# Optimization experiments

Measured on AMD Instinct MI355X. Metric: run time of the kernel, lower is better.

## Reference

```python
import jax, jax.numpy as jnp
import numpy as np

# Phi-2 config
B, S = 4, 1024            # batch, seq_len (uniform prefill)
T = B * S                 # total tokens
HID = 2560
H = 32                    # attention heads
D = HID // H              # head_size = 80
ROT = int(0.4 * D)        # partial rotary dim = 32
THETA = 10000.0
SCALE = D ** -0.5
NUM_SLOTS = 2 * T


def setup_inputs() -> dict:
    key = jax.random.key(0)
    ks = jax.random.split(key, 6)
    hidden_states = jax.random.normal(ks[0], (T, HID), jnp.float32) * 0.02
    # true rope tables: positions restart per sequence
    pos = jnp.tile(jnp.arange(S, dtype=jnp.float32), B)                 # [T]
    inv_freq = 1.0 / (THETA ** (jnp.arange(0, ROT, 2, dtype=jnp.float32) / ROT))  # [ROT/2]
    freqs = pos[:, None] * inv_freq[None, :]                            # [T, ROT/2]
    cos, sin = jnp.cos(freqs), jnp.sin(freqs)
    slots = jnp.arange(T, dtype=jnp.int32)
    kv_cache_k = jnp.zeros((NUM_SLOTS, H, D), jnp.float32)
    kv_cache_v = jnp.zeros((NUM_SLOTS, H, D), jnp.float32)
    qkv_w = jax.random.normal(ks[1], (3 * HID, HID), jnp.float32) * 0.02
    qkv_b = jax.random.normal(ks[2], (3 * HID,), jnp.float32) * 0.02
    dense_w = jax.random.normal(ks[3], (HID, HID), jnp.float32) * 0.02
    dense_b = jax.random.normal(ks[4], (HID,), jnp.float32) * 0.02
    return {"hidden_states": hidden_states, "cos": cos, "sin": sin, "slots": slots,
            "kv_cache_k": kv_cache_k, "kv_cache_v": kv_cache_v,
            "qkv_w": qkv_w, "qkv_b": qkv_b, "dense_w": dense_w, "dense_b": dense_b}


def _partial_rope(x, cos, sin):
    # x: [T, H, D]; rotate-half rope on the first ROT dims only
    x1 = x[..., : ROT // 2]
    x2 = x[..., ROT // 2 : ROT]
    c = cos[:, None, :]  # [T,1,ROT/2]
    s = sin[:, None, :]
    rot = jnp.concatenate([x1 * c - x2 * s, x1 * s + x2 * c], axis=-1)
    return jnp.concatenate([rot, x[..., ROT:]], axis=-1)


def reference(hidden_states, cos, sin, slots, kv_cache_k, kv_cache_v,
              qkv_w, qkv_b, dense_w, dense_b):
    # fused QKV projection
    qkv = hidden_states @ qkv_w.T + qkv_b                 # [T, 3*HID]
    q = qkv[:, :HID].reshape(T, H, D)
    k = qkv[:, HID:2 * HID].reshape(T, H, D)
    v = qkv[:, 2 * HID:].reshape(T, H, D)
    # partial rotary on q and k
    q = _partial_rope(q, cos, sin)
    k = _partial_rope(k, cos, sin)
    # KV-cache write (reshape_and_cache)
    kc = kv_cache_k.at[slots].set(k)
    vc = kv_cache_v.at[slots].set(v)
    # causal flash-attention (prefill path), uniform seq lengths
    qb = q.reshape(B, S, H, D)
    kb = k.reshape(B, S, H, D)
    vb = v.reshape(B, S, H, D)
    scores = jnp.einsum("bqhd,bkhd->bhqk", qb, kb) * SCALE  # [B,H,S,S]
    causal = jnp.tril(jnp.ones((S, S), bool))
    scores = jnp.where(causal[None, None], scores, jnp.finfo(scores.dtype).min)
    probs = jax.nn.softmax(scores, axis=-1)
    attn = jnp.einsum("bhqk,bkhd->bqhd", probs, vb).reshape(T, HID)
    out = attn @ dense_w.T + dense_b                       # [T, HID]
    return out, kc, vc
```

## Files before the change

### kernel.cpp

```cpp
#include <hip/hip_runtime.h>

#define SEQ    1024
#define NBAT   4
#define TTOK   4096
#define HIDN   2560
#define NQKV   7680
#define NHEAD  32
#define DHEAD  80
#define NSLOT  8192
#define SCALE_F 0.111803398874989485f
#define LOG2E_F 1.4426950408889634f

typedef float  f32x4  __attribute__((ext_vector_type(4)));
typedef __bf16 bf16x8 __attribute__((ext_vector_type(8)));
typedef short  s16x8  __attribute__((ext_vector_type(8)));
typedef short  s16x4  __attribute__((ext_vector_type(4)));
typedef ushort u16x4  __attribute__((ext_vector_type(4)));

typedef __attribute__((address_space(3))) void lds_v;
typedef __attribute__((address_space(1))) void glb_v;

__device__ __forceinline__ void gload16(const void* g, void* l) {
  __builtin_amdgcn_global_load_lds((glb_v*)g, (lds_v*)l, 16, 0, 0);
}

__device__ __forceinline__ f32x4 mfma16(s16x8 a, s16x8 b, f32x4 c) {
  return __builtin_amdgcn_mfma_f32_16x16x32_bf16(
      __builtin_bit_cast(bf16x8, a), __builtin_bit_cast(bf16x8, b), c, 0, 0, 0);
}

__device__ __forceinline__ ushort f2bf(float f) {
  uint u = __builtin_bit_cast(uint, f);
  u += 0x7fffu + ((u >> 16) & 1u);
  return (ushort)(u >> 16);
}
__device__ __forceinline__ float bf2f(ushort h) {
  uint u = (uint)h << 16;
  return __builtin_bit_cast(float, u);
}

#define NQ_HS  2621440
#define NQ_QW  4915200
#define NQ_DW  1638400
#define NQ_ALL (NQ_HS + NQ_QW + NQ_DW)
__global__ __launch_bounds__(256)
void prep_kernel(const float* __restrict__ hs, const float* __restrict__ qkvw,
                 const float* __restrict__ densew,
                 ushort* __restrict__ hsb, ushort* __restrict__ qkvwb,
                 ushort* __restrict__ densewb, uint* __restrict__ flags) {
  const int tid0 = blockIdx.x * 256 + threadIdx.x;
  if (tid0 < NSLOT) flags[tid0] = 0u;
  const int stride = gridDim.x * 256;
  for (int i = tid0; i < NQ_ALL; i += stride) {
    const float* src; ushort* dst; int q;
    if (i < NQ_HS)              { src = hs;     dst = hsb;     q = i; }
    else if (i < NQ_HS + NQ_QW) { src = qkvw;   dst = qkvwb;   q = i - NQ_HS; }
    else                        { src = densew; dst = densewb; q = i - NQ_HS - NQ_QW; }
    float4 v = *(const float4*)(src + q * 4);
    u16x4 o = { f2bf(v.x), f2bf(v.y), f2bf(v.z), f2bf(v.w) };
    *(u16x4*)(dst + q * 4) = o;
  }
}

template<int OUT_BF16>
__global__ __launch_bounds__(512, 2)
void gemm8p(const ushort* __restrict__ A, const ushort* __restrict__ B,
            const float* __restrict__ bias, void* __restrict__ Cout,
            int M, int N, int K, int GX, int RR, int RC) {
  __shared__ ushort sA[3][256 * 64];
  __shared__ ushort sB[2][256 * 64];
  const int tid = threadIdx.x;
  const int l   = tid & 63;
  const int w   = tid >> 6;
  const int wm  = w >> 2, wn = w & 3;
  const int r   = l & 15,  g = l >> 4;

  const int fl  = blockIdx.x;
  const int xcd = fl & 7;
  const int idx = fl >> 3;
  const int cgroups = GX / RC;
  const int rg = xcd / cgroups, cg = xcd % cgroups;
  const int by = rg * RR + idx / RC;
  const int bx = cg * RC + idx % RC;
  const int m0  = by * 256, n0 = bx * 256;
  const int NT  = K >> 6;

  const int srow = w * 16 + (l >> 3);
  const int scol = ((l & 7) ^ (l >> 3)) * 8;
  const ushort* Ab = A + (size_t)(m0 + srow) * K + scol;
  const ushort* Bb = B + (size_t)(n0 + srow) * K + scol;
  const size_t r8   = (size_t)8 * K;
  const size_t r128 = (size_t)128 * K;

#define STG_A(t_, h_, buf_) { \
    const ushort* gp = Ab + (size_t)(t_) * 64 + (size_t)(h_) * r128; \
    char* lp = (char*)(&sA[buf_][0]) + ((h_) * 128 + w * 16) * 128; \
    gload16(gp, lp); gload16(gp + r8, lp + 1024); }
#define STG_B(t_, h_, buf_) { \
    const ushort* gp = Bb + (size_t)(t_) * 64 + (size_t)(h_) * r128; \
    char* lp = (char*)(&sB[buf_][0]) + ((h_) * 128 + w * 16) * 128; \
    gload16(gp, lp); gload16(gp + r8, lp + 1024); }

  const int kswz = (r & 7) * 8;
  const int c0 = (g * 8) ^ kswz;
  const int c1 = (32 + g * 8) ^ kswz;
  const int arow = (wm * 128 + r) * 64;
  const int brow = (wn * 64 + r) * 64;

  f32x4 acc[8][4];
#pragma unroll
  for (int m = 0; m < 8; m++)
#pragma unroll
    for (int n = 0; n < 4; n++) { f32x4 z = {0.f,0.f,0.f,0.f}; acc[m][n] = z; }

  STG_A(0, 0, 0); STG_A(0, 1, 0);
  STG_B(0, 0, 0); STG_B(0, 1, 0);
  STG_A(1, 0, 1); STG_A(1, 1, 1);
  asm volatile("s_waitcnt vmcnt(4)" ::: "memory");
  __builtin_amdgcn_sched_barrier(0);
  __builtin_amdgcn_s_barrier();

#define MFMA_Q(q_) \
    __builtin_amdgcn_s_setprio(1); \
    _Pragma("unroll") \
    for (int n = 0; n < 4; n++) acc[2*(q_)  ][n] = mfma16(x0, b0[n], acc[2*(q_)  ][n]); \
    _Pragma("unroll") \
    for (int n = 0; n < 4; n++) acc[2*(q_)+1][n] = mfma16(y0, b0[n], acc[2*(q_)+1][n]); \
    _Pragma("unroll") \
    for (int n = 0; n < 4; n++) acc[2*(q_)  ][n] = mfma16(x1, b1[n], acc[2*(q_)  ][n]); \
    _Pragma("unroll") \
    for (int n = 0; n < 4; n++) acc[2*(q_)+1][n] = mfma16(y1, b1[n], acc[2*(q_)+1][n]); \
    __builtin_amdgcn_s_setprio(0);

#define LOAD_A(m0_, m1_) \
    x0 = *(const s16x8*)&cA[arow + (m0_) * 1024 + c0]; \
    x1 = *(const s16x8*)&cA[arow + (m0_) * 1024 + c1]; \
    y0 = *(const s16x8*)&cA[arow + (m1_) * 1024 + c0]; \
    y1 = *(const s16x8*)&cA[arow + (m1_) * 1024 + c1];

  int bA = 0;
#pragma unroll 1
  for (int t = 0; t < NT; ++t) {
    const ushort* cA = &sA[bA][0];
    const ushort* cB = &sB[t & 1][0];
    const int nb = (t & 1) ^ 1;
    int a2 = bA + 2; if (a2 >= 3) a2 -= 3;

    s16x8 b0[4], b1[4], x0, x1, y0, y1;

#pragma unroll
    for (int n = 0; n < 4; n++) {
      b0[n] = *(const s16x8*)&cB[brow + n * 1024 + c0];
      b1[n] = *(const s16x8*)&cB[brow + n * 1024 + c1];
    }
    LOAD_A(0, 1)
    if (t + 1 < NT) STG_B(t + 1, 0, nb);
    __builtin_amdgcn_s_barrier();
    MFMA_Q(0)
    __builtin_amdgcn_s_barrier();

    LOAD_A(2, 3)
    if (t + 1 < NT) STG_B(t + 1, 1, nb);
    __builtin_amdgcn_s_barrier();
    MFMA_Q(1)
    __builtin_amdgcn_s_barrier();

    LOAD_A(4, 5)
    if (t + 2 < NT) STG_A(t + 2, 0, a2);
    __builtin_amdgcn_s_barrier();
    MFMA_Q(2)
    __builtin_amdgcn_s_barrier();

    LOAD_A(6, 7)
    if (t + 2 < NT) STG_A(t + 2, 1, a2);
    __builtin_amdgcn_s_barrier();
    MFMA_Q(3)
    if (t < NT - 2) {
      asm volatile("s_waitcnt vmcnt(4)" ::: "memory");
    } else if (t == NT - 2) {
      asm volatile("s_waitcnt vmcnt(0)" ::: "memory");
    }
    __builtin_amdgcn_sched_barrier(0);
    __builtin_amdgcn_s_barrier();

    bA++; if (bA >= 3) bA = 0;
  }

#pragma unroll
  for (int n = 0; n < 4; n++) {
    const int col = n0 + wn * 64 + n * 16 + r;
    const float bv = bias[col];
#pragma unroll
    for (int m = 0; m < 8; m++) {
      const int row = m0 + wm * 128 + m * 16 + g * 4;
#pragma unroll
      for (int j = 0; j < 4; j++) {
        float v = acc[m][n][j] + bv;
        if (OUT_BF16) ((ushort*)Cout)[(size_t)(row + j) * N + col] = f2bf(v);
        else          ((float*)Cout)[(size_t)(row + j) * N + col] = v;
      }
    }
  }
#undef STG_A
#undef STG_B
#undef MFMA_Q
#undef LOAD_A
}

template<int OUT_BF16>
__global__ __launch_bounds__(256)
void gemm_nt(const ushort* __restrict__ A, const ushort* __restrict__ B,
             const float* __restrict__ bias, void* __restrict__ Cout,
             int M, int N, int K, int GX, int RR, int RC) {
  __shared__ ushort lsA[128 * 32];
  __shared__ ushort lsB[128 * 32];
  const int tid  = threadIdx.x;
  const int lane = tid & 63;
  const int w    = tid >> 6;
  const int wr   = w >> 1, wc = w & 1;
  const int r    = lane & 15, g = lane >> 4;

  const int fl  = blockIdx.x;
  const int xcd = fl & 7;
  const int idx = fl >> 3;
  const int cgroups = GX / RC;
  const int rg = xcd / cgroups, cg = xcd % cgroups;
  const int by = rg * RR + idx / RC;
  const int bx = cg * RC + idx % RC;
  const int m0 = by * 128, n0 = bx * 128;

  const int row0 = tid >> 2;
  const int kc0  = (tid & 3) * 8;

  f32x4 acc[4][4];
#pragma unroll
  for (int i = 0; i < 4; i++)
#pragma unroll
    for (int j = 0; j < 4; j++) { f32x4 z = {0.f,0.f,0.f,0.f}; acc[i][j] = z; }

  const ushort* Abase = A + (size_t)m0 * K;
  const ushort* Bbase = B + (size_t)n0 * K;
  char* dstA0 = (char*)lsA + (size_t)(w * 64) * 16;
  char* dstA1 = (char*)lsA + (size_t)(256 + w * 64) * 16;
  char* dstB0 = (char*)lsB + (size_t)(w * 64) * 16;
  char* dstB1 = (char*)lsB + (size_t)(256 + w * 64) * 16;

  for (int k0 = 0; k0 < K; k0 += 32) {
    gload16(Abase + (size_t)row0 * K + k0 + kc0,        dstA0);
    gload16(Abase + (size_t)(64 + row0) * K + k0 + kc0, dstA1);
    gload16(Bbase + (size_t)row0 * K + k0 + kc0,        dstB0);
    gload16(Bbase + (size_t)(64 + row0) * K + k0 + kc0, dstB1);
    __syncthreads();

    s16x8 af[4], bfr[4];
#pragma unroll
    for (int f = 0; f < 4; f++) {
      af[f]  = *(const s16x8*)&lsA[(wr * 64 + f * 16 + r) * 32 + g * 8];
      bfr[f] = *(const s16x8*)&lsB[(wc * 64 + f * 16 + r) * 32 + g * 8];
    }
#pragma unroll
    for (int fi = 0; fi < 4; fi++)
#pragma unroll
      for (int fj = 0; fj < 4; fj++)
        acc[fi][fj] = mfma16(af[fi], bfr[fj], acc[fi][fj]);
    __syncthreads();
  }

#pragma unroll
  for (int fj = 0; fj < 4; fj++) {
    const int col = n0 + wc * 64 + fj * 16 + r;
    const float bv = bias[col];
#pragma unroll
    for (int fi = 0; fi < 4; fi++) {
      const int row = m0 + wr * 64 + fi * 16 + g * 4;
#pragma unroll
      for (int j = 0; j < 4; j++) {
        float v = acc[fi][fj][j] + bv;
        if (OUT_BF16) ((ushort*)Cout)[(size_t)(row + j) * N + col] = f2bf(v);
        else          ((float*)Cout)[(size_t)(row + j) * N + col] = v;
      }
    }
  }
}

__global__ __launch_bounds__(256)
void rope_scatter(ushort* __restrict__ qkv, const float* __restrict__ cosp,
                  const float* __restrict__ sinp, const int* __restrict__ slots,
                  float* __restrict__ kc, float* __restrict__ vc,
                  uint* __restrict__ flags) {
  const int t = blockIdx.x;
  const int tid = threadIdx.x;
  __shared__ float cs[16], sn[16];
  if (tid < 16)       cs[tid]      = cosp[t * 16 + tid];
  else if (tid < 32)  sn[tid - 16] = sinp[t * 16 + tid - 16];
  __syncthreads();
  const int slot = slots[t];
  if (tid == 0) flags[slot] = 1u;
  ushort* qrow = qkv + (size_t)t * NQKV;
  float* kcr = kc + (size_t)slot * HIDN;
  float* vcr = vc + (size_t)slot * HIDN;

  for (int idx = tid; idx < 512; idx += 256) {
    int hh = idx >> 4, i = idx & 15;
    ushort* p = qrow + hh * DHEAD + i;
    float x1 = bf2f(p[0]), x2 = bf2f(p[16]);
    float c = cs[i], s = sn[i];
    p[0]  = f2bf(x1 * c - x2 * s);
    p[16] = f2bf(x1 * s + x2 * c);
  }
  for (int idx = tid; idx < 512; idx += 256) {
    int hh = idx >> 4, i = idx & 15;
    ushort* p = qrow + HIDN + hh * DHEAD + i;
    float x1 = bf2f(p[0]), x2 = bf2f(p[16]);
    float c = cs[i], s = sn[i];
    float k1 = x1 * c - x2 * s, k2 = x1 * s + x2 * c;
    p[0]  = f2bf(k1);
    p[16] = f2bf(k2);
    kcr[hh * DHEAD + i]      = k1;
    kcr[hh * DHEAD + i + 16] = k2;
  }
  for (int idx = tid; idx < 1536; idx += 256) {
    int hh = idx / 48, d = 32 + idx % 48;
    kcr[hh * DHEAD + d] = bf2f(qrow[HIDN + hh * DHEAD + d]);
  }
  for (int idx = tid; idx < HIDN; idx += 256) {
    vcr[idx] = bf2f(qrow[2 * HIDN + idx]);
  }
}

__global__ __launch_bounds__(256)
void cache_fill(const float* __restrict__ kin, const float* __restrict__ vin,
                const uint* __restrict__ f,
                float* __restrict__ kout, float* __restrict__ vout) {
  const int row = blockIdx.x;
  if (f[row]) return;
  const float4* ks = (const float4*)(kin + (size_t)row * HIDN);
  const float4* vs = (const float4*)(vin + (size_t)row * HIDN);
  float4* kd = (float4*)(kout + (size_t)row * HIDN);
  float4* vd = (float4*)(vout + (size_t)row * HIDN);
  for (int i = threadIdx.x; i < HIDN / 4; i += 256) { kd[i] = ks[i]; vd[i] = vs[i]; }
}

__global__ __launch_bounds__(512, 4)
void attn_kernel(const ushort* __restrict__ qkv, ushort* __restrict__ attn_out) {
  const int qb = 7 - blockIdx.y;
  const int hb = blockIdx.x;
  const int h = hb & 31, b = hb >> 5;
  __shared__ ushort lsK[64 * 104];
  __shared__ ushort lsVT[80 * 68];
  __shared__ ushort lsP[8][16 * 68];
  const int tid  = threadIdx.x;
  const int lane = tid & 63, w = tid >> 6;
  const int r    = lane & 15, g = lane >> 4;

  {
    int kv = tid >> 3, cp = tid & 7;
    *(uint*)&lsK[kv * 104 + 80 + cp * 2] = 0u;
  }

  const size_t qrow = (size_t)(b * SEQ + qb * 128 + w * 16 + r);
  const ushort* qp = qkv + qrow * NQKV + h * DHEAD;
  s16x8 qf[3];
  qf[0] = *(const s16x8*)(qp + g * 8);
  qf[1] = *(const s16x8*)(qp + 32 + g * 8);
  if (g < 2) qf[2] = *(const s16x8*)(qp + 64 + g * 8);
  else { s16x8 z = {0,0,0,0,0,0,0,0}; qf[2] = z; }

  int off_g[5]; uint off_kv[5];
#pragma unroll
  for (int j = 0; j < 5; j++) {
    int i = tid + j * 512;
    int kv = i / 40, dp = i - kv * 40;
    off_g[j]  = kv * NQKV + dp * 2;
    off_kv[j] = (uint)(kv * 104 + dp * 2) | ((uint)(dp * 2 * 68 + kv) << 16);
  }
  const ushort* kvbase = qkv + (size_t)(b * SEQ) * NQKV + HIDN + h * DHEAD;

  uint kreg[5], vreg[5];
#pragma unroll
  for (int j = 0; j < 5; j++) {
    kreg[j] = *(const uint*)(kvbase + off_g[j]);
    vreg[j] = *(const uint*)(kvbase + off_g[j] + HIDN);
  }

  float m_run[4] = {-1e30f, -1e30f, -1e30f, -1e30f};
  float l_run[4] = {0.f, 0.f, 0.f, 0.f};
  f32x4 acco[5];
#pragma unroll
  for (int nb = 0; nb < 5; nb++) { f32x4 z = {0.f,0.f,0.f,0.f}; acco[nb] = z; }

  const int ntiles = 2 * qb + 2;
  for (int t = 0; t < ntiles; t++) {
#pragma unroll
    for (int j = 0; j < 5; j++) {
      int ok = off_kv[j] & 0xffff, ov = off_kv[j] >> 16;
      *(uint*)&lsK[ok] = kreg[j];
      uint vv = vreg[j];
      lsVT[ov]      = (ushort)(vv & 0xffffu);
      lsVT[ov + 68] = (ushort)(vv >> 16);
    }
    __syncthreads();

    if (t + 1 < ntiles) {
      const ushort* nb_ = kvbase + (size_t)(t + 1) * 64 * NQKV;
#pragma unroll
      for (int j = 0; j < 5; j++) {
        kreg[j] = *(const uint*)(nb_ + off_g[j]);
        vreg[j] = *(const uint*)(nb_ + off_g[j] + HIDN);
      }
    }

    f32x4 sacc[4];
#pragma unroll
    for (int cb = 0; cb < 4; cb++) {
      f32x4 acc = {0.f, 0.f, 0.f, 0.f};
#pragma unroll
      for (int c = 0; c < 3; c++) {
        s16x8 kf = *(const s16x8*)&lsK[(cb * 16 + r) * 104 + c * 32 + g * 8];
        acc = mfma16(qf[c], kf, acc);
      }
      sacc[cb] = acc;
    }

    const bool diag = (t >= 2 * qb);
    const int kv0 = t * 64;
    const int q0  = qb * 128 + w * 16 + g * 4;
#pragma unroll
    for (int cb = 0; cb < 4; cb++)
#pragma unroll
      for (int j = 0; j < 4; j++) {
        float s = sacc[cb][j] * SCALE_F;
        if (diag && (kv0 + cb * 16 + r) > (q0 + j)) s = -1e30f;
        sacc[cb][j] = s;
      }

    float mnew[4], alpha[4], rs[4];
#pragma unroll
    for (int j = 0; j < 4; j++) {
      float m = fmaxf(fmaxf(sacc[0][j], sacc[1][j]), fmaxf(sacc[2][j], sacc[3][j]));
      m = fmaxf(m, __shfl_xor(m, 1));
      m = fmaxf(m, __shfl_xor(m, 2));
      m = fmaxf(m, __shfl_xor(m, 4));
      m = fmaxf(m, __shfl_xor(m, 8));
      mnew[j]  = fmaxf(m_run[j], m);
      alpha[j] = exp2f((m_run[j] - mnew[j]) * LOG2E_F);
      m_run[j] = mnew[j];
      rs[j] = 0.f;
    }

#pragma unroll
    for (int cb = 0; cb < 4; cb++)
#pragma unroll
      for (int j = 0; j < 4; j++) {
        float p = exp2f((sacc[cb][j] - mnew[j]) * LOG2E_F);
        rs[j] += p;
        lsP[w][(g * 4 + j) * 68 + cb * 16 + r] = f2bf(p);
      }

#pragma unroll
    for (int j = 0; j < 4; j++) {
      float v = rs[j];
      v += __shfl_xor(v, 1);
      v += __shfl_xor(v, 2);
      v += __shfl_xor(v, 4);
      v += __shfl_xor(v, 8);
      l_run[j] = l_run[j] * alpha[j] + v;
#pragma unroll
      for (int nb = 0; nb < 5; nb++) acco[nb][j] *= alpha[j];
    }

    s16x8 pa[2];
#pragma unroll
    for (int ch = 0; ch < 2; ch++) {
      s16x4 lo = *(const s16x4*)&lsP[w][r * 68 + ch * 32 + g * 8];
      s16x4 hi = *(const s16x4*)&lsP[w][r * 68 + ch * 32 + g * 8 + 4];
      pa[ch] = __builtin_shufflevector(lo, hi, 0, 1, 2, 3, 4, 5, 6, 7);
    }

#pragma unroll
    for (int nb = 0; nb < 5; nb++)
#pragma unroll
      for (int ch = 0; ch < 2; ch++) {
        s16x4 lo = *(const s16x4*)&lsVT[(nb * 16 + r) * 68 + ch * 32 + g * 8];
        s16x4 hi = *(const s16x4*)&lsVT[(nb * 16 + r) * 68 + ch * 32 + g * 8 + 4];
        s16x8 vf = __builtin_shufflevector(lo, hi, 0, 1, 2, 3, 4, 5, 6, 7);
        acco[nb] = mfma16(pa[ch], vf, acco[nb]);
      }

    __syncthreads();
  }

  const size_t orow = (size_t)(b * SEQ + qb * 128 + w * 16 + g * 4);
#pragma unroll
  for (int j = 0; j < 4; j++) {
    float inv = 1.0f / l_run[j];
#pragma unroll
    for (int nb = 0; nb < 5; nb++)
      attn_out[(orow + j) * HIDN + h * DHEAD + nb * 16 + r] = f2bf(acco[nb][j] * inv);
  }
}

extern "C" void kernel_launch(void* const* d_in, const int* in_sizes, int n_in,
                              void* d_out, int out_size, void* d_ws, size_t ws_size,
                              hipStream_t stream) {
  (void)in_sizes; (void)n_in; (void)out_size; (void)ws_size;
  const float* hs      = (const float*)d_in[0];
  const float* cosp    = (const float*)d_in[1];
  const float* sinp    = (const float*)d_in[2];
  const int*   slots   = (const int*)  d_in[3];
  const float* kck_in  = (const float*)d_in[4];
  const float* kcv_in  = (const float*)d_in[5];
  const float* qkvw    = (const float*)d_in[6];
  const float* qkvb    = (const float*)d_in[7];
  const float* densew  = (const float*)d_in[8];
  const float* denseb  = (const float*)d_in[9];

  float* out    = (float*)d_out;
  float* kc_out = out + (size_t)TTOK * HIDN;
  float* vc_out = kc_out + (size_t)NSLOT * HIDN;

  char* ws = (char*)d_ws;
  ushort* hsb     = (ushort*)(ws);
  ushort* qkvwb   = (ushort*)(ws + 20971520);
  ushort* densewb = (ushort*)(ws + 60293120);
  ushort* qkvb16  = (ushort*)(ws + 73400320);
  ushort* attnb   = (ushort*)(ws + 136314880);
  uint*   flags   = (uint*)(ws + 136314880);

  prep_kernel<<<2048, 256, 0, stream>>>(hs, qkvw, densew, hsb, qkvwb, densewb, flags);

  gemm8p<1><<<480, 512, 0, stream>>>(hsb, qkvwb, qkvb, qkvb16, TTOK, NQKV, HIDN, 30, 4, 15);

  rope_scatter<<<TTOK, 256, 0, stream>>>(qkvb16, cosp, sinp, slots, kc_out, vc_out, flags);

  cache_fill<<<NSLOT, 256, 0, stream>>>(kck_in, kcv_in, flags, kc_out, vc_out);

  attn_kernel<<<dim3(NHEAD * NBAT, SEQ / 128), 512, 0, stream>>>(qkvb16, attnb);

  gemm_nt<0><<<640, 256, 0, stream>>>(
      attnb, densewb, denseb, out, TTOK, HIDN, HIDN, 20, 8, 10);
}
```

Measured before the change: 440.7 us.

## Merge cache fill and dense weight conversion into attention launch

```diff
diff --git a/kernel.cpp b/kernel.cpp
--- a/kernel.cpp
+++ b/kernel.cpp
@@ -42,20 +42,18 @@
 #define NQ_HS  2621440
 #define NQ_QW  4915200
 #define NQ_DW  1638400
-#define NQ_ALL (NQ_HS + NQ_QW + NQ_DW)
+#define NQ_PRE (NQ_HS + NQ_QW)
 __global__ __launch_bounds__(256)
 void prep_kernel(const float* __restrict__ hs, const float* __restrict__ qkvw,
-                 const float* __restrict__ densew,
                  ushort* __restrict__ hsb, ushort* __restrict__ qkvwb,
-                 ushort* __restrict__ densewb, uint* __restrict__ flags) {
+                 uint* __restrict__ flags) {
   const int tid0 = blockIdx.x * 256 + threadIdx.x;
   if (tid0 < NSLOT) flags[tid0] = 0u;
   const int stride = gridDim.x * 256;
-  for (int i = tid0; i < NQ_ALL; i += stride) {
+  for (int i = tid0; i < NQ_PRE; i += stride) {
     const float* src; ushort* dst; int q;
-    if (i < NQ_HS)              { src = hs;     dst = hsb;     q = i; }
-    else if (i < NQ_HS + NQ_QW) { src = qkvw;   dst = qkvwb;   q = i - NQ_HS; }
-    else                        { src = densew; dst = densewb; q = i - NQ_HS - NQ_QW; }
+    if (i < NQ_HS) { src = hs;   dst = hsb;   q = i; }
+    else           { src = qkvw; dst = qkvwb; q = i - NQ_HS; }
     float4 v = *(const float4*)(src + q * 4);
     u16x4 o = { f2bf(v.x), f2bf(v.y), f2bf(v.z), f2bf(v.w) };
     *(u16x4*)(dst + q * 4) = o;
@@ -328,27 +326,41 @@
   }
 }
 
-__global__ __launch_bounds__(256)
-void cache_fill(const float* __restrict__ kin, const float* __restrict__ vin,
-                const uint* __restrict__ f,
-                float* __restrict__ kout, float* __restrict__ vout) {
-  const int row = blockIdx.x;
-  if (f[row]) return;
-  const float4* ks = (const float4*)(kin + (size_t)row * HIDN);
-  const float4* vs = (const float4*)(vin + (size_t)row * HIDN);
-  float4* kd = (float4*)(kout + (size_t)row * HIDN);
-  float4* vd = (float4*)(vout + (size_t)row * HIDN);
-  for (int i = threadIdx.x; i < HIDN / 4; i += 256) { kd[i] = ks[i]; vd[i] = vs[i]; }
-}
-
 __global__ __launch_bounds__(512, 4)
-void attn_kernel(const ushort* __restrict__ qkv, ushort* __restrict__ attn_out) {
-  const int qb = 7 - blockIdx.y;
-  const int hb = blockIdx.x;
-  const int h = hb & 31, b = hb >> 5;
+void mega_kernel(const ushort* __restrict__ qkv, ushort* __restrict__ attn_out,
+                 const float* __restrict__ kin, const float* __restrict__ vin,
+                 const uint* __restrict__ flags,
+                 float* __restrict__ kout, float* __restrict__ vout,
+                 const float* __restrict__ densew, ushort* __restrict__ densewb) {
   __shared__ ushort lsK[64 * 104];
   __shared__ ushort lsVT[80 * 68];
   __shared__ ushort lsP[8][16 * 68];
+  const int bid = blockIdx.x;
+
+  if (bid >= 1024) {
+    if (bid < 5120) {
+      const int row = (bid - 1024) * 2 + (threadIdx.x >> 8);
+      const int t2  = threadIdx.x & 255;
+      if (flags[row]) return;
+      const float4* ks = (const float4*)(kin + (size_t)row * HIDN);
+      const float4* vs = (const float4*)(vin + (size_t)row * HIDN);
+      float4* kd = (float4*)(kout + (size_t)row * HIDN);
+      float4* vd = (float4*)(vout + (size_t)row * HIDN);
+      for (int i = t2; i < HIDN / 4; i += 256) { kd[i] = ks[i]; vd[i] = vs[i]; }
+    } else {
+      int i = (bid - 5120) * 512 + threadIdx.x;
+      for (; i < NQ_DW; i += 256 * 512) {
+        float4 v = *(const float4*)(densew + i * 4);
+        u16x4 o = { f2bf(v.x), f2bf(v.y), f2bf(v.z), f2bf(v.w) };
+        *(u16x4*)(densewb + i * 4) = o;
+      }
+    }
+    return;
+  }
+
+  const int qb = 7 - (bid >> 7);
+  const int hb = bid & 127;
+  const int h = hb & 31, b = hb >> 5;
   const int tid  = threadIdx.x;
   const int lane = tid & 63, w = tid >> 6;
   const int r    = lane & 15, g = lane >> 4;
@@ -521,21 +533,20 @@
 
   char* ws = (char*)d_ws;
   ushort* hsb     = (ushort*)(ws);
+  ushort* attnb   = (ushort*)(ws);
   ushort* qkvwb   = (ushort*)(ws + 20971520);
   ushort* densewb = (ushort*)(ws + 60293120);
   ushort* qkvb16  = (ushort*)(ws + 73400320);
-  ushort* attnb   = (ushort*)(ws + 136314880);
   uint*   flags   = (uint*)(ws + 136314880);
 
-  prep_kernel<<<2048, 256, 0, stream>>>(hs, qkvw, densew, hsb, qkvwb, densewb, flags);
+  prep_kernel<<<2048, 256, 0, stream>>>(hs, qkvw, hsb, qkvwb, flags);
 
   gemm8p<1><<<480, 512, 0, stream>>>(hsb, qkvwb, qkvb, qkvb16, TTOK, NQKV, HIDN, 30, 4, 15);
 
   rope_scatter<<<TTOK, 256, 0, stream>>>(qkvb16, cosp, sinp, slots, kc_out, vc_out, flags);
 
-  cache_fill<<<NSLOT, 256, 0, stream>>>(kck_in, kcv_in, flags, kc_out, vc_out);
-
-  attn_kernel<<<dim3(NHEAD * NBAT, SEQ / 128), 512, 0, stream>>>(qkvb16, attnb);
+  mega_kernel<<<5376, 512, 0, stream>>>(qkvb16, attnb, kck_in, kcv_in, flags,
+                                        kc_out, vc_out, densew, densewb);
 
   gemm_nt<0><<<640, 256, 0, stream>>>(
       attnb, densewb, denseb, out, TTOK, HIDN, HIDN, 20, 8, 10);
```

After: 433.4 us. About the same (-1.7%).
